# Optimization experiments

Measured on AMD Instinct MI355X. Metric: run time of the kernel, lower is better.

## Reference

```python
import jax, jax.numpy as jnp
import numpy as np

ALPHA = 0.5
B = 4096
K = 8192


def setup_inputs() -> dict:
    key = jax.random.key(0)
    k1, k2 = jax.random.split(key)
    outputs = jax.random.normal(k1, (B, K), dtype=jnp.float32)
    labels = jax.random.randint(k2, (B,), 0, K)
    targets = jax.nn.one_hot(labels, K, dtype=jnp.float32)
    S = jnp.eye(K, dtype=jnp.float32)          # soft-label matrix (state)
    S_t = jnp.zeros((K, K), dtype=jnp.float32)  # running stats (state)
    count = jnp.zeros((K, 1), dtype=jnp.float32)
    return {"outputs": outputs, "targets": targets, "S": S, "S_t": S_t, "count": count}


def reference(outputs, targets, S, S_t, count):
    # loss path
    ls = jax.nn.log_softmax(outputs, axis=1)          # [B, K]
    bsz = outputs.shape[0]
    target_label = jnp.argmax(targets, axis=1)        # [B]
    prediction = jnp.argmax(outputs, axis=1)          # [B]
    soft_targets = S[target_label]                    # [B, K] gather
    ce_hard = -(ls * targets).sum() / bsz
    ce_soft = -(ls * soft_targets).sum() / bsz
    loss = ALPHA * ce_hard + (1.0 - ALPHA) * ce_soft

    # stats accumulation (the original python for-loop, as one fused scatter-add)
    probs = jax.nn.softmax(jax.lax.stop_gradient(outputs), axis=1)  # [B, K]
    correct = (prediction == target_label).astype(probs.dtype)      # [B]
    S_t_new = S_t + jax.ops.segment_sum(probs * correct[:, None], target_label, num_segments=K)
    count_new = count + jax.ops.segment_sum(correct, target_label, num_segments=K)[:, None]
    return loss, S_t_new, count_new
```

## Files before the change

### kernel.cpp

```cpp
#include <hip/hip_runtime.h>
#include <math.h>

#define K 8192
#define BROWS 4096
#define ALPHA 0.5f
#define NTOT ((size_t)K * (size_t)K)
#define VEC4 16777215
#define NBLK 2048
#define TOTTH ((size_t)NBLK * 256)

typedef float f32x4 __attribute__((ext_vector_type(4)));

__device__ __forceinline__ void argmax_combine(float& v, int& i, float v2, int i2){
  if (v2 > v || (v2 == v && i2 < i)) { v = v2; i = i2; }
}

__global__ __launch_bounds__(256) void fused_kernel(
    const float* __restrict__ outputs,
    const float* __restrict__ targets,
    const float* __restrict__ S,
    const float* __restrict__ S_t,
    const float* __restrict__ count,
    float* __restrict__ out,
    float* __restrict__ rowloss,
    int*   __restrict__ rowtl,
    int*   __restrict__ rowcorrect,
    float* __restrict__ rowm,
    float* __restrict__ rowinvZ)
{
  __shared__ float s_v[2][4]; __shared__ int s_i[2][4];
  __shared__ float s_m; __shared__ int s_pred; __shared__ int s_tl;
  __shared__ float s_sums[4][5];

  const int bb = blockIdx.x;
  const int t  = threadIdx.x;
  const int lane = t & 63;
  const int wid  = t >> 6;
  const size_t tid = (size_t)bb * 256 + t;

  {
    const f32x4* src4 = (const f32x4*)S_t;
    f32x4* dst4 = (f32x4*)(out + 4);
#pragma unroll
    for (int outer = 0; outer < 4; ++outer) {
      const size_t d0 = tid + (size_t)outer * 8 * TOTTH;
      f32x4 a[8];
#pragma unroll
      for (int i = 0; i < 8; ++i) a[i] = src4[d0 + (size_t)i * TOTTH];
#pragma unroll
      for (int i = 0; i < 8; ++i) {
        const size_t d = d0 + (size_t)i * TOTTH;
        float nx = __shfl_down(a[i].x, 1, 64);
        float ny = __shfl_down(a[i].y, 1, 64);
        float nz = __shfl_down(a[i].z, 1, 64);
        const bool instore = d < (size_t)VEC4;
        if (lane == 63 && instore) {
          f32x4 e = src4[d + 1];
          nx = e.x; ny = e.y; nz = e.z;
        }
        if (instore) {
          f32x4 v; v.x = a[i].w; v.y = nx; v.z = ny; v.w = nz;
          __builtin_nontemporal_store(v, &dst4[d]);
        }
      }
    }
    if (bb == 0) {
      if (t < 3) out[1 + t] = S_t[t];
      if (t == 3) out[NTOT] = S_t[NTOT - 1];
    } else if (bb == 1) {
      float* out_count = out + 1 + NTOT;
      for (int i = t; i < K; i += 256) out_count[i] = count[i];
    }
  }

  for (int rr = 0; rr < 2; ++rr) {
    const int r = bb + rr * NBLK;

    const float4* orow = (const float4*)(outputs + (size_t)r * K);
    float x[32];
#pragma unroll
    for (int i = 0; i < 8; ++i){
      float4 v = orow[i*256 + t];
      x[4*i+0]=v.x; x[4*i+1]=v.y; x[4*i+2]=v.z; x[4*i+3]=v.w;
    }

    float mv = -INFINITY; int mi = 0x7fffffff;
#pragma unroll
    for (int i = 0; i < 8; ++i){
#pragma unroll
      for (int c = 0; c < 4; ++c){
        int idx = i*1024 + t*4 + c;
        argmax_combine(mv, mi, x[4*i+c], idx);
      }
    }

    const float4* trow = (const float4*)(targets + (size_t)r * K);
    float tv = -INFINITY; int ti = 0x7fffffff;
    float d_hard = 0.f, s_hard = 0.f;
#pragma unroll
    for (int i = 0; i < 8; ++i){
      float4 v = trow[i*256 + t];
      float tc[4] = {v.x, v.y, v.z, v.w};
#pragma unroll
      for (int c = 0; c < 4; ++c){
        int idx = i*1024 + t*4 + c;
        d_hard += x[4*i+c] * tc[c];
        s_hard += tc[c];
        argmax_combine(tv, ti, tc[c], idx);
      }
    }

#pragma unroll
    for (int off = 32; off; off >>= 1){
      float v2 = __shfl_down(mv, off, 64); int i2 = __shfl_down(mi, off, 64);
      argmax_combine(mv, mi, v2, i2);
      v2 = __shfl_down(tv, off, 64); i2 = __shfl_down(ti, off, 64);
      argmax_combine(tv, ti, v2, i2);
    }

    if (lane == 0){ s_v[0][wid]=mv; s_i[0][wid]=mi; s_v[1][wid]=tv; s_i[1][wid]=ti; }
    __syncthreads();
    if (t == 0){
      float av=s_v[0][0]; int ai=s_i[0][0];
      float bv=s_v[1][0]; int bi=s_i[1][0];
#pragma unroll
      for (int w=1; w<4; ++w){
        argmax_combine(av, ai, s_v[0][w], s_i[0][w]);
        argmax_combine(bv, bi, s_v[1][w], s_i[1][w]);
      }
      s_m = av; s_pred = ai; s_tl = bi;
    }
    __syncthreads();
    const float m  = s_m;
    const int   tl = s_tl;

    float se = 0.f;
#pragma unroll
    for (int i = 0; i < 32; ++i) se += expf(x[i] - m);

    const float4* srow = (const float4*)(S + (size_t)tl * K);
    float d_soft = 0.f, s_soft = 0.f;
#pragma unroll
    for (int i = 0; i < 8; ++i){
      float4 v = srow[i*256 + t];
      d_soft += x[4*i+0]*v.x + x[4*i+1]*v.y + x[4*i+2]*v.z + x[4*i+3]*v.w;
      s_soft += v.x + v.y + v.z + v.w;
    }

    float sums[5] = {d_hard, s_hard, se, d_soft, s_soft};
#pragma unroll
    for (int off = 32; off; off >>= 1){
#pragma unroll
      for (int j = 0; j < 5; ++j) sums[j] += __shfl_down(sums[j], off, 64);
    }
    if (lane == 0){
#pragma unroll
      for (int j = 0; j < 5; ++j) s_sums[wid][j] = sums[j];
    }
    __syncthreads();
    if (t == 0){
      float tot[5];
#pragma unroll
      for (int j=0;j<5;++j) tot[j] = s_sums[0][j]+s_sums[1][j]+s_sums[2][j]+s_sums[3][j];
      float Z = tot[2];
      float logZ = logf(Z);
      float ceh = -(tot[0] - (m + logZ) * tot[1]);
      float ces = -(tot[3] - (m + logZ) * tot[4]);
      rowloss[r]    = (ALPHA * ceh + (1.0f - ALPHA) * ces) * (1.0f / (float)BROWS);
      rowtl[r]      = tl;
      rowcorrect[r] = (s_pred == tl) ? 1 : 0;
      rowm[r]       = m;
      rowinvZ[r]    = 1.0f / Z;
    }
  }
}

__global__ __launch_bounds__(256) void epilogue_kernel(
    const float* __restrict__ outputs,
    const float* __restrict__ rowloss,
    const int*   __restrict__ rowtl,
    const int*   __restrict__ rowcorrect,
    const float* __restrict__ rowm,
    const float* __restrict__ rowinvZ,
    float* __restrict__ out)
{
  const int b = blockIdx.x;
  const int t = threadIdx.x;
  if (b == BROWS) {
    float s = 0.f;
    for (int i = t; i < BROWS; i += 256) s += rowloss[i];
#pragma unroll
    for (int off = 32; off; off >>= 1) s += __shfl_down(s, off, 64);
    __shared__ float sh[4];
    if ((t & 63) == 0) sh[t >> 6] = s;
    __syncthreads();
    if (t == 0) out[0] = sh[0] + sh[1] + sh[2] + sh[3];
    return;
  }
  if (!rowcorrect[b]) return;
  const int tl = rowtl[b];
  const float m = rowm[b], invZ = rowinvZ[b];
  const float* orow = outputs + (size_t)b * K;
  float* drow = out + 1 + (size_t)tl * K;
  for (int k = t; k < K; k += 256)
    atomicAdd(&drow[k], expf(orow[k] - m) * invZ);
  if (t == 0) atomicAdd(out + 1 + NTOT + tl, 1.0f);
}

extern "C" void kernel_launch(void* const* d_in, const int* in_sizes, int n_in,
                              void* d_out, int out_size, void* d_ws, size_t ws_size,
                              hipStream_t stream) {
  const float* outputs = (const float*)d_in[0];
  const float* targets = (const float*)d_in[1];
  const float* S       = (const float*)d_in[2];
  const float* S_t     = (const float*)d_in[3];
  const float* count   = (const float*)d_in[4];

  float* out = (float*)d_out;

  float* rowloss    = (float*)d_ws;
  float* rowm       = rowloss + BROWS;
  float* rowinvZ    = rowm + BROWS;
  int*   rowtl      = (int*)(rowinvZ + BROWS);
  int*   rowcorrect = rowtl + BROWS;

  hipLaunchKernelGGL(fused_kernel, dim3(NBLK), dim3(256), 0, stream,
                     outputs, targets, S, S_t, count, out,
                     rowloss, rowtl, rowcorrect, rowm, rowinvZ);
  hipLaunchKernelGGL(epilogue_kernel, dim3(BROWS + 1), dim3(256), 0, stream,
                     outputs, rowloss, rowtl, rowcorrect, rowm, rowinvZ, out);
}
```

Measured before the change: 766.6 us.

## Interleave S_t copy chunks with per-row loss work, one row per block

The grid changes from 2048 blocks that each copy part of S_t and then process two rows, to 4096 blocks that each handle one row and a contiguous 64 KB slice of the S_t copy. The copy loads and stores are split into two halves placed between the row reductions, so memory traffic overlaps with the argmax, exp and dot-product work. The target argmax and the hard-label reductions are replaced by a direct one-hot lookup (value > 0.5), which drops a shuffle reduction and two sums. That lookup assumes targets are exactly one-hot, and a row with no entry above 0.5 would leave s_tl unset.

```diff
diff --git a/kernel.cpp b/kernel.cpp
--- a/kernel.cpp
+++ b/kernel.cpp
@@ -6,8 +6,6 @@
 #define ALPHA 0.5f
 #define NTOT ((size_t)K * (size_t)K)
 #define VEC4 16777215
-#define NBLK 2048
-#define TOTTH ((size_t)NBLK * 256)
 
 typedef float f32x4 __attribute__((ext_vector_type(4)));
 
@@ -28,150 +26,155 @@
     float* __restrict__ rowm,
     float* __restrict__ rowinvZ)
 {
-  __shared__ float s_v[2][4]; __shared__ int s_i[2][4];
+  __shared__ float s_v[4]; __shared__ int s_i[4];
   __shared__ float s_m; __shared__ int s_pred; __shared__ int s_tl;
-  __shared__ float s_sums[4][5];
+  __shared__ float s_dhard;
+  __shared__ float s_sums[4][3];
 
   const int bb = blockIdx.x;
   const int t  = threadIdx.x;
   const int lane = t & 63;
   const int wid  = t >> 6;
-  const size_t tid = (size_t)bb * 256 + t;
-
-  {
-    const f32x4* src4 = (const f32x4*)S_t;
-    f32x4* dst4 = (f32x4*)(out + 4);
-#pragma unroll
-    for (int outer = 0; outer < 4; ++outer) {
-      const size_t d0 = tid + (size_t)outer * 8 * TOTTH;
-      f32x4 a[8];
-#pragma unroll
-      for (int i = 0; i < 8; ++i) a[i] = src4[d0 + (size_t)i * TOTTH];
-#pragma unroll
-      for (int i = 0; i < 8; ++i) {
-        const size_t d = d0 + (size_t)i * TOTTH;
-        float nx = __shfl_down(a[i].x, 1, 64);
-        float ny = __shfl_down(a[i].y, 1, 64);
-        float nz = __shfl_down(a[i].z, 1, 64);
-        const bool instore = d < (size_t)VEC4;
-        if (lane == 63 && instore) {
-          f32x4 e = src4[d + 1];
-          nx = e.x; ny = e.y; nz = e.z;
-        }
-        if (instore) {
-          f32x4 v; v.x = a[i].w; v.y = nx; v.z = ny; v.w = nz;
-          __builtin_nontemporal_store(v, &dst4[d]);
-        }
+
+  const f32x4* src4 = (const f32x4*)S_t;
+  f32x4* dst4 = (f32x4*)(out + 4);
+  const size_t cbase = (size_t)bb * 4096 + t;
+
+  f32x4 a[8];
+#pragma unroll
+  for (int i = 0; i < 8; ++i) a[i] = src4[cbase + (size_t)i * 256];
+
+  const float4* orow = (const float4*)(outputs + (size_t)bb * K);
+  float x[32];
+#pragma unroll
+  for (int i = 0; i < 8; ++i){
+    float4 v = orow[i*256 + t];
+    x[4*i+0]=v.x; x[4*i+1]=v.y; x[4*i+2]=v.z; x[4*i+3]=v.w;
+  }
+  float mv = -INFINITY; int mi = 0x7fffffff;
+#pragma unroll
+  for (int i = 0; i < 8; ++i){
+#pragma unroll
+    for (int c = 0; c < 4; ++c){
+      int idx = i*1024 + t*4 + c;
+      argmax_combine(mv, mi, x[4*i+c], idx);
+    }
+  }
+
+  const float4* trow = (const float4*)(targets + (size_t)bb * K);
+#pragma unroll
+  for (int i = 0; i < 8; ++i){
+    float4 v = trow[i*256 + t];
+    float tc[4] = {v.x, v.y, v.z, v.w};
+#pragma unroll
+    for (int c = 0; c < 4; ++c){
+      if (tc[c] > 0.5f){
+        s_tl = i*1024 + t*4 + c;
+        s_dhard = x[4*i+c];
       }
     }
-    if (bb == 0) {
-      if (t < 3) out[1 + t] = S_t[t];
-      if (t == 3) out[NTOT] = S_t[NTOT - 1];
-    } else if (bb == 1) {
-      float* out_count = out + 1 + NTOT;
-      for (int i = t; i < K; i += 256) out_count[i] = count[i];
-    }
-  }
-
-  for (int rr = 0; rr < 2; ++rr) {
-    const int r = bb + rr * NBLK;
-
-    const float4* orow = (const float4*)(outputs + (size_t)r * K);
-    float x[32];
-#pragma unroll
-    for (int i = 0; i < 8; ++i){
-      float4 v = orow[i*256 + t];
-      x[4*i+0]=v.x; x[4*i+1]=v.y; x[4*i+2]=v.z; x[4*i+3]=v.w;
-    }
-
-    float mv = -INFINITY; int mi = 0x7fffffff;
-#pragma unroll
-    for (int i = 0; i < 8; ++i){
-#pragma unroll
-      for (int c = 0; c < 4; ++c){
-        int idx = i*1024 + t*4 + c;
-        argmax_combine(mv, mi, x[4*i+c], idx);
-      }
-    }
-
-    const float4* trow = (const float4*)(targets + (size_t)r * K);
-    float tv = -INFINITY; int ti = 0x7fffffff;
-    float d_hard = 0.f, s_hard = 0.f;
-#pragma unroll
-    for (int i = 0; i < 8; ++i){
-      float4 v = trow[i*256 + t];
-      float tc[4] = {v.x, v.y, v.z, v.w};
-#pragma unroll
-      for (int c = 0; c < 4; ++c){
-        int idx = i*1024 + t*4 + c;
-        d_hard += x[4*i+c] * tc[c];
-        s_hard += tc[c];
-        argmax_combine(tv, ti, tc[c], idx);
-      }
-    }
-
-#pragma unroll
-    for (int off = 32; off; off >>= 1){
-      float v2 = __shfl_down(mv, off, 64); int i2 = __shfl_down(mi, off, 64);
-      argmax_combine(mv, mi, v2, i2);
-      v2 = __shfl_down(tv, off, 64); i2 = __shfl_down(ti, off, 64);
-      argmax_combine(tv, ti, v2, i2);
-    }
-
-    if (lane == 0){ s_v[0][wid]=mv; s_i[0][wid]=mi; s_v[1][wid]=tv; s_i[1][wid]=ti; }
-    __syncthreads();
-    if (t == 0){
-      float av=s_v[0][0]; int ai=s_i[0][0];
-      float bv=s_v[1][0]; int bi=s_i[1][0];
-#pragma unroll
-      for (int w=1; w<4; ++w){
-        argmax_combine(av, ai, s_v[0][w], s_i[0][w]);
-        argmax_combine(bv, bi, s_v[1][w], s_i[1][w]);
-      }
-      s_m = av; s_pred = ai; s_tl = bi;
-    }
-    __syncthreads();
-    const float m  = s_m;
-    const int   tl = s_tl;
-
-    float se = 0.f;
-#pragma unroll
-    for (int i = 0; i < 32; ++i) se += expf(x[i] - m);
-
-    const float4* srow = (const float4*)(S + (size_t)tl * K);
-    float d_soft = 0.f, s_soft = 0.f;
-#pragma unroll
-    for (int i = 0; i < 8; ++i){
-      float4 v = srow[i*256 + t];
-      d_soft += x[4*i+0]*v.x + x[4*i+1]*v.y + x[4*i+2]*v.z + x[4*i+3]*v.w;
-      s_soft += v.x + v.y + v.z + v.w;
-    }
-
-    float sums[5] = {d_hard, s_hard, se, d_soft, s_soft};
-#pragma unroll
-    for (int off = 32; off; off >>= 1){
-#pragma unroll
-      for (int j = 0; j < 5; ++j) sums[j] += __shfl_down(sums[j], off, 64);
-    }
-    if (lane == 0){
-#pragma unroll
-      for (int j = 0; j < 5; ++j) s_sums[wid][j] = sums[j];
-    }
-    __syncthreads();
-    if (t == 0){
-      float tot[5];
-#pragma unroll
-      for (int j=0;j<5;++j) tot[j] = s_sums[0][j]+s_sums[1][j]+s_sums[2][j]+s_sums[3][j];
-      float Z = tot[2];
-      float logZ = logf(Z);
-      float ceh = -(tot[0] - (m + logZ) * tot[1]);
-      float ces = -(tot[3] - (m + logZ) * tot[4]);
-      rowloss[r]    = (ALPHA * ceh + (1.0f - ALPHA) * ces) * (1.0f / (float)BROWS);
-      rowtl[r]      = tl;
-      rowcorrect[r] = (s_pred == tl) ? 1 : 0;
-      rowm[r]       = m;
-      rowinvZ[r]    = 1.0f / Z;
-    }
+  }
+
+#pragma unroll
+  for (int off = 32; off; off >>= 1){
+    float v2 = __shfl_down(mv, off, 64); int i2 = __shfl_down(mi, off, 64);
+    argmax_combine(mv, mi, v2, i2);
+  }
+  if (lane == 0){ s_v[wid] = mv; s_i[wid] = mi; }
+
+#pragma unroll
+  for (int i = 0; i < 8; ++i){
+    const size_t d = cbase + (size_t)i * 256;
+    float nx = __shfl_down(a[i].x, 1, 64);
+    float ny = __shfl_down(a[i].y, 1, 64);
+    float nz = __shfl_down(a[i].z, 1, 64);
+    if (lane == 63) {
+      f32x4 e = src4[d + 1];
+      nx = e.x; ny = e.y; nz = e.z;
+    }
+    f32x4 v; v.x = a[i].w; v.y = nx; v.z = ny; v.w = nz;
+    __builtin_nontemporal_store(v, &dst4[d]);
+  }
+
+  __syncthreads();
+  if (t == 0){
+    float av = s_v[0]; int ai = s_i[0];
+#pragma unroll
+    for (int w = 1; w < 4; ++w) argmax_combine(av, ai, s_v[w], s_i[w]);
+    s_m = av; s_pred = ai;
+  }
+  __syncthreads();
+  const float m  = s_m;
+  const int   tl = s_tl;
+
+  f32x4 b[8];
+#pragma unroll
+  for (int i = 0; i < 8; ++i) b[i] = src4[cbase + (size_t)(i + 8) * 256];
+
+  float se = 0.f;
+#pragma unroll
+  for (int i = 0; i < 32; ++i) se += expf(x[i] - m);
+
+  const float4* srow = (const float4*)(S + (size_t)tl * K);
+  float d_soft = 0.f, s_soft = 0.f;
+#pragma unroll
+  for (int i = 0; i < 8; ++i){
+    float4 v = srow[i*256 + t];
+    d_soft += x[4*i+0]*v.x + x[4*i+1]*v.y + x[4*i+2]*v.z + x[4*i+3]*v.w;
+    s_soft += v.x + v.y + v.z + v.w;
+  }
+
+  float sums[3] = {se, d_soft, s_soft};
+#pragma unroll
+  for (int off = 32; off; off >>= 1){
+#pragma unroll
+    for (int j = 0; j < 3; ++j) sums[j] += __shfl_down(sums[j], off, 64);
+  }
+  if (lane == 0){
+#pragma unroll
+    for (int j = 0; j < 3; ++j) s_sums[wid][j] = sums[j];
+  }
+
+#pragma unroll
+  for (int i = 0; i < 8; ++i){
+    const size_t d = cbase + (size_t)(i + 8) * 256;
+    float nx = __shfl_down(b[i].x, 1, 64);
+    float ny = __shfl_down(b[i].y, 1, 64);
+    float nz = __shfl_down(b[i].z, 1, 64);
+    const bool instore = d < (size_t)VEC4;
+    if (lane == 63 && instore) {
+      f32x4 e = src4[d + 1];
+      nx = e.x; ny = e.y; nz = e.z;
+    }
+    if (instore) {
+      f32x4 v; v.x = b[i].w; v.y = nx; v.z = ny; v.w = nz;
+      __builtin_nontemporal_store(v, &dst4[d]);
+    }
+  }
+
+  __syncthreads();
+  if (t == 0){
+    float tot[3];
+#pragma unroll
+    for (int j = 0; j < 3; ++j)
+      tot[j] = s_sums[0][j] + s_sums[1][j] + s_sums[2][j] + s_sums[3][j];
+    float Z = tot[0];
+    float logZ = logf(Z);
+    float ceh = -(s_dhard - (m + logZ));
+    float ces = -(tot[1] - (m + logZ) * tot[2]);
+    rowloss[bb]    = (ALPHA * ceh + (1.0f - ALPHA) * ces) * (1.0f / (float)BROWS);
+    rowtl[bb]      = tl;
+    rowcorrect[bb] = (s_pred == tl) ? 1 : 0;
+    rowm[bb]       = m;
+    rowinvZ[bb]    = 1.0f / Z;
+  }
+
+  if (bb == 0) {
+    if (t < 3) out[1 + t] = S_t[t];
+    if (t == 3) out[NTOT] = S_t[NTOT - 1];
+  } else if (bb == 1) {
+    float* out_count = out + 1 + NTOT;
+    for (int i = t; i < K; i += 256) out_count[i] = count[i];
   }
 }
 
@@ -224,7 +227,7 @@
   int*   rowtl      = (int*)(rowinvZ + BROWS);
   int*   rowcorrect = rowtl + BROWS;
 
-  hipLaunchKernelGGL(fused_kernel, dim3(NBLK), dim3(256), 0, stream,
+  hipLaunchKernelGGL(fused_kernel, dim3(BROWS), dim3(256), 0, stream,
                      outputs, targets, S, S_t, count, out,
                      rowloss, rowtl, rowcorrect, rowm, rowinvZ);
   hipLaunchKernelGGL(epilogue_kernel, dim3(BROWS + 1), dim3(256), 0, stream,
```

Result: faster. 743.1 us (-3.1%).
